# Kernel optimization log

Hardware: AMD Instinct MI355X
Metric: run time of the kernel (lower is better)

Reference implementation:

```python
import jax, jax.numpy as jnp
import numpy as np

N = 50000      # movie nodes
E = 1000000    # edges per metapath
F_IN = 512
HID = 128
HEADS = 8
D = HID // HEADS  # 16
OUT = 3
NEG_SLOPE = 0.2   # PyG HANConv leaky_relu slope


def setup_inputs() -> dict:
    key = jax.random.key(0)
    ks = jax.random.split(key, 16)
    x = jax.random.normal(ks[0], (N, F_IN), jnp.float32)
    ei0 = jax.random.randint(ks[1], (2, E), 0, N, jnp.int32)
    ei1 = jax.random.randint(ks[2], (2, E), 0, N, jnp.int32)
    W_proj = jax.random.normal(ks[3], (F_IN, HID), jnp.float32) / np.sqrt(F_IN)
    b_proj = jnp.zeros((HID,), jnp.float32)
    att_src0 = jax.random.normal(ks[4], (HEADS, D), jnp.float32) / np.sqrt(D)
    att_dst0 = jax.random.normal(ks[5], (HEADS, D), jnp.float32) / np.sqrt(D)
    att_src1 = jax.random.normal(ks[6], (HEADS, D), jnp.float32) / np.sqrt(D)
    att_dst1 = jax.random.normal(ks[7], (HEADS, D), jnp.float32) / np.sqrt(D)
    Wk = jax.random.normal(ks[8], (HID, HID), jnp.float32) / np.sqrt(HID)
    bk = jnp.zeros((HID,), jnp.float32)
    q = jax.random.normal(ks[9], (HID,), jnp.float32) / np.sqrt(HID)
    W_lin = jax.random.normal(ks[10], (HID, OUT), jnp.float32) / np.sqrt(HID)
    b_lin = jnp.zeros((OUT,), jnp.float32)
    return dict(x=x, edge_index_mp0=ei0, edge_index_mp1=ei1,
                W_proj=W_proj, b_proj=b_proj,
                att_src0=att_src0, att_dst0=att_dst0,
                att_src1=att_src1, att_dst1=att_dst1,
                Wk=Wk, bk=bk, q=q, W_lin=W_lin, b_lin=b_lin)


def _han_edge_type(xp, src, dst, att_src, att_dst):
    """Node-level multi-head attention for one metapath (eval mode, no dropout).
    xp: [N, H, D] projected features; src/dst: [E] indices.
    """
    a_src = jnp.einsum('nhd,hd->nh', xp, att_src)  # [N, H]
    a_dst = jnp.einsum('nhd,hd->nh', xp, att_dst)
    alpha = jax.nn.leaky_relu(a_src[src] + a_dst[dst], NEG_SLOPE)  # [E, H]
    # segment softmax over incoming edges of each dst node
    amax = jax.ops.segment_max(alpha, dst, num_segments=N)
    amax = jnp.where(jnp.isfinite(amax), amax, 0.0)
    ex = jnp.exp(alpha - amax[dst])
    denom = jax.ops.segment_sum(ex, dst, num_segments=N)
    w = ex / (denom[dst] + 1e-16)                 # [E, H]
    msg = w[:, :, None] * xp[src]                 # [E, H, D]
    out = jax.ops.segment_sum(msg, dst, num_segments=N)  # [N, H, D]
    return jax.nn.relu(out.reshape(N, HID))


def reference(x, edge_index_mp0, edge_index_mp1, W_proj, b_proj,
              att_src0, att_dst0, att_src1, att_dst1,
              Wk, bk, q, W_lin, b_lin):
    xp = (x @ W_proj + b_proj).reshape(N, HEADS, D)
    o0 = _han_edge_type(xp, edge_index_mp0[0], edge_index_mp0[1], att_src0, att_dst0)
    o1 = _han_edge_type(xp, edge_index_mp1[0], edge_index_mp1[1], att_src1, att_dst1)
    outs = jnp.stack([o0, o1], axis=0)            # [M=2, N, HID]
    # semantic-level attention: score_m = sum(q * mean_n tanh(k_lin(o_m)))
    scores = jnp.einsum('mh,h->m', jnp.tanh(outs @ Wk + bk).mean(axis=1), q)
    beta = jax.nn.softmax(scores)                 # [2]
    fused = jnp.einsum('m,mnh->nh', beta, outs)   # [N, HID]
    return fused @ W_lin + b_lin                  # [N, OUT]
```

## Files before the change

kernel.cpp:

```cpp
#include <hip/hip_runtime.h>
#include <hip/hip_bf16.h>

#define NN 50000
#define EE 1000000
#define FIN 512
#define HIDDEN 128
#define NH 8
#define DH 16
#define NOUT 3
#define NBUCK 196
#define EPB 8192
#define NBLKA ((EE + EPB - 1) / EPB)

typedef unsigned short u16;
typedef unsigned int u32;
typedef __attribute__((ext_vector_type(8))) short short8;
typedef __attribute__((ext_vector_type(4))) float f32x4;

__device__ __forceinline__ float b2f(u16 b) { return __uint_as_float(((u32)b) << 16); }
__device__ __forceinline__ u16 f2b(float f) { return (u16)(__float_as_uint(f) >> 16); }
__device__ __forceinline__ u16 f2b_rne(float f) {
    u32 u = __float_as_uint(f);
    return (u16)((u + 0x7FFFu + ((u >> 16) & 1u)) >> 16);
}

__device__ __forceinline__ void gload16(const u16* g, u16* l) {
    __builtin_amdgcn_global_load_lds(
        (const __attribute__((address_space(1))) unsigned int*)(g),
        (__attribute__((address_space(3))) unsigned int*)(l), 16, 0, 0);
}

#define W_WP   0
#define W_BP   65536
#define W_AS0  65664
#define W_AD0  65792
#define W_AS1  65920
#define W_AD1  66048
#define W_WK   66176
#define W_BK   82560
#define W_Q    82688
#define W_WL   82816
#define W_BL   83200
#define W_TOT  83203

__global__ void k_detect(const void* __restrict__ x, int* __restrict__ flag)
{
    const u16* xb = (const u16*)x;
    int t = threadIdx.x;
    int insane = 0;
    #pragma unroll
    for (int i = 0; i < 16; ++i) {
        int idx = ((t * 16 + i) * 131) * 2;
        float v = b2f(xb[idx]);
        float a = fabsf(v);
        bool sane = (a == 0.0f) || (a >= 1e-8f && a <= 1e4f);
        insane += sane ? 0 : 1;
    }
    __shared__ int red[256];
    red[t] = insane;
    __syncthreads();
    for (int s = 128; s > 0; s >>= 1) { if (t < s) red[t] += red[t + s]; __syncthreads(); }
    if (t == 0) flag[0] = (red[0] > 1024) ? 1 : 0;
}

__global__ __launch_bounds__(256) void k_convert(
    const void* Wp, const void* bp, const void* as0, const void* ad0,
    const void* as1, const void* ad1, const void* Wk, const void* bk,
    const void* q, const void* Wl, const void* bl,
    const int* __restrict__ flag, float* __restrict__ W)
{
    int i = blockIdx.x * 256 + threadIdx.x;
    if (i >= W_TOT) return;
    const void* src; int off;
    if      (i < W_BP)  { src = Wp;  off = i; }
    else if (i < W_AS0) { src = bp;  off = i - W_BP; }
    else if (i < W_AD0) { src = as0; off = i - W_AS0; }
    else if (i < W_AS1) { src = ad0; off = i - W_AD0; }
    else if (i < W_AD1) { src = as1; off = i - W_AS1; }
    else if (i < W_WK)  { src = ad1; off = i - W_AD1; }
    else if (i < W_BK)  { src = Wk;  off = i - W_WK; }
    else if (i < W_Q)   { src = bk;  off = i - W_BK; }
    else if (i < W_WL)  { src = q;   off = i - W_Q; }
    else if (i < W_BL)  { src = Wl;  off = i - W_WL; }
    else                { src = bl;  off = i - W_BL; }
    float v = flag[0] ? ((const float*)src)[off] : b2f(((const u16*)src)[off]);
    W[i] = v;
}

#define PREPN (FIN*HIDDEN + HIDDEN*HIDDEN)
__global__ __launch_bounds__(256) void k_prepw(
    const float* __restrict__ Wpf, const float* __restrict__ Wkf,
    u16* __restrict__ WhiT, u16* __restrict__ WloT, u16* __restrict__ WkThi)
{
    int idx = blockIdx.x*256 + threadIdx.x;
    if (idx >= PREPN) return;
    if (idx < FIN*HIDDEN) {
        int k = idx >> 7, n = idx & 127;
        float w = Wpf[idx];
        u32 hb = __float_as_uint(w) & 0xFFFF0000u;
        WhiT[(size_t)n*FIN + k] = (u16)(hb >> 16);
        WloT[(size_t)n*FIN + k] = f2b(w - __uint_as_float(hb));
    } else {
        int i = idx - FIN*HIDDEN;
        int k = i >> 7, h = i & 127;
        WkThi[(size_t)h*HIDDEN + k] = f2b_rne(Wkf[i]);
    }
}

__global__ __launch_bounds__(256) void k_projm_f32(
    const void* __restrict__ xv, const u16* __restrict__ WhiT,
    const u16* __restrict__ WloT, const float* __restrict__ bpf,
    const int* __restrict__ flag, u16* __restrict__ xpb)
{
    if (!flag[0]) return;
    __shared__ u16 lds[2][16384];
    const int t = threadIdx.x;
    const int lane = t & 63;
    const int wid = t >> 6;
    const int m16 = lane & 15;
    const int quad = lane >> 4;
    const int wr = wid >> 1, wc = wid & 1;
    const int blockRow = blockIdx.x * 128;
    const float* xf = (const float*)xv;

    const int srow = t >> 1;
    const int shalf = t & 1;
    int gxrow = blockRow + srow; if (gxrow >= NN) gxrow = NN - 1;
    const float* xr = xf + (size_t)gxrow * FIN + shalf * 16;
    const int ssw = (srow >> 1) & 3;
    const int aw0 = srow*32 + ((shalf*2)     ^ ssw) * 8;
    const int aw1 = srow*32 + ((shalf*2 + 1) ^ ssw) * 8;

    int bp0 = t, bp1 = t + 256;
    int br0 = bp0 >> 2, br1 = bp1 >> 2;
    int bc0 = (bp0 & 3) ^ ((br0 >> 1) & 3);
    int bc1 = (bp1 & 3) ^ ((br1 >> 1) & 3);
    const u16* srcBh0 = WhiT + (size_t)br0 * FIN + bc0 * 8;
    const u16* srcBh1 = WhiT + (size_t)br1 * FIN + bc1 * 8;
    const u16* srcBl0 = WloT + (size_t)br0 * FIN + bc0 * 8;
    const u16* srcBl1 = WloT + (size_t)br1 * FIN + bc1 * 8;
    const int dB0 = bp0 * 8, dB1 = bp1 * 8;

    int aoff[4], boff[4];
    #pragma unroll
    for (int mt = 0; mt < 4; ++mt) {
        int r = wr*64 + mt*16 + m16;
        aoff[mt] = r*32 + ((quad ^ ((r >> 1) & 3)) << 3);
    }
    #pragma unroll
    for (int nt = 0; nt < 4; ++nt) {
        int r = wc*64 + nt*16 + m16;
        boff[nt] = r*32 + ((quad ^ ((r >> 1) & 3)) << 3);
    }

    f32x4 acc[4][4];
    #pragma unroll
    for (int i = 0; i < 4; ++i)
        #pragma unroll
        for (int j = 0; j < 4; ++j) acc[i][j] = (f32x4)(0.f);

    u16* Lc = lds[0];
    u16* Ln = lds[1];

    {
        float4 v0 = *(const float4*)(xr);
        float4 v1 = *(const float4*)(xr + 4);
        float4 v2 = *(const float4*)(xr + 8);
        float4 v3 = *(const float4*)(xr + 12);
        gload16(srcBh0, Lc + 8192  + dB0);
        gload16(srcBh1, Lc + 8192  + dB1);
        gload16(srcBl0, Lc + 12288 + dB0);
        gload16(srcBl1, Lc + 12288 + dB1);
        float xs[16] = {v0.x,v0.y,v0.z,v0.w, v1.x,v1.y,v1.z,v1.w,
                        v2.x,v2.y,v2.z,v2.w, v3.x,v3.y,v3.z,v3.w};
        short8 h0, h1, l0, l1;
        #pragma unroll
        for (int j = 0; j < 8; ++j) {
            u32 u = __float_as_uint(xs[j]);   u32 hb = u & 0xFFFF0000u;
            h0[j] = (short)(hb >> 16); l0[j] = (short)f2b(xs[j] - __uint_as_float(hb));
            u32 u2 = __float_as_uint(xs[8+j]); u32 hb2 = u2 & 0xFFFF0000u;
            h1[j] = (short)(hb2 >> 16); l1[j] = (short)f2b(xs[8+j] - __uint_as_float(hb2));
        }
        *(short8*)(Lc + aw0) = h0;
        *(short8*)(Lc + aw1) = h1;
        *(short8*)(Lc + 4096 + aw0) = l0;
        *(short8*)(Lc + 4096 + aw1) = l1;
    }
    __syncthreads();

    #pragma unroll 1
    for (int ks = 0; ks < 16; ++ks) {
        const int kt = (ks + 1) * 32;
        float4 v0, v1, v2, v3;
        if (ks < 15) {
            v0 = *(const float4*)(xr + kt);
            v1 = *(const float4*)(xr + kt + 4);
            v2 = *(const float4*)(xr + kt + 8);
            v3 = *(const float4*)(xr + kt + 12);
            gload16(srcBh0 + kt, Ln + 8192  + dB0);
            gload16(srcBh1 + kt, Ln + 8192  + dB1);
            gload16(srcBl0 + kt, Ln + 12288 + dB0);
            gload16(srcBl1 + kt, Ln + 12288 + dB1);
        }
        short8 bh[4], bl[4];
        #pragma unroll
        for (int nt = 0; nt < 4; ++nt) {
            bh[nt] = *(const short8*)(Lc + 8192  + boff[nt]);
            bl[nt] = *(const short8*)(Lc + 12288 + boff[nt]);
        }
        #pragma unroll
        for (int mt = 0; mt < 4; ++mt) {
            short8 ah = *(const short8*)(Lc + aoff[mt]);
            short8 al = *(const short8*)(Lc + 4096 + aoff[mt]);
            #pragma unroll
            for (int nt = 0; nt < 4; ++nt) {
                acc[mt][nt] = __builtin_amdgcn_mfma_f32_16x16x32_bf16(ah, bh[nt], acc[mt][nt], 0,0,0);
                acc[mt][nt] = __builtin_amdgcn_mfma_f32_16x16x32_bf16(ah, bl[nt], acc[mt][nt], 0,0,0);
                acc[mt][nt] = __builtin_amdgcn_mfma_f32_16x16x32_bf16(al, bh[nt], acc[mt][nt], 0,0,0);
            }
        }
        if (ks < 15) {
            float xs[16] = {v0.x,v0.y,v0.z,v0.w, v1.x,v1.y,v1.z,v1.w,
                            v2.x,v2.y,v2.z,v2.w, v3.x,v3.y,v3.z,v3.w};
            short8 h0, h1, l0, l1;
            #pragma unroll
            for (int j = 0; j < 8; ++j) {
                u32 u = __float_as_uint(xs[j]);   u32 hb = u & 0xFFFF0000u;
                h0[j] = (short)(hb >> 16); l0[j] = (short)f2b(xs[j] - __uint_as_float(hb));
                u32 u2 = __float_as_uint(xs[8+j]); u32 hb2 = u2 & 0xFFFF0000u;
                h1[j] = (short)(hb2 >> 16); l1[j] = (short)f2b(xs[8+j] - __uint_as_float(hb2));
            }
            *(short8*)(Ln + aw0) = h0;
            *(short8*)(Ln + aw1) = h1;
            *(short8*)(Ln + 4096 + aw0) = l0;
            *(short8*)(Ln + 4096 + aw1) = l1;
        }
        __syncthreads();
        u16* tmp = Lc; Lc = Ln; Ln = tmp;
    }

    #pragma unroll
    for (int nt = 0; nt < 4; ++nt) {
        int col = wc*64 + nt*16 + m16;
        float bias = bpf[col];
        #pragma unroll
        for (int mt = 0; mt < 4; ++mt) {
            int orow0 = blockRow + wr*64 + mt*16 + quad*4;
            #pragma unroll
            for (int r = 0; r < 4; ++r) {
                int orow = orow0 + r;
                if (orow < NN) xpb[(size_t)orow*HIDDEN + col] = f2b_rne(acc[mt][nt][r] + bias);
            }
        }
    }
}

__global__ __launch_bounds__(256) void k_projm_bf16(
    const void* __restrict__ x, const u16* __restrict__ WhiT,
    const u16* __restrict__ WloT, const float* __restrict__ bpf,
    const int* __restrict__ flag, u16* __restrict__ xpb)
{
    if (flag[0]) return;
    __shared__ u16 lds[2][12288];
    const int t = threadIdx.x;
    const int lane = t & 63;
    const int wid = t >> 6;
    const int m16 = lane & 15;
    const int quad = lane >> 4;
    const int wr = wid >> 1, wc = wid & 1;
    const int blockRow = blockIdx.x * 128;
    const u16* xb = (const u16*)x;

    const int r0 = t >> 2,         c0 = (t & 3) * 8;
    const int r1 = (t + 256) >> 2, c1 = ((t + 256) & 3) * 8;
    int g0 = blockRow + r0; if (g0 >= NN) g0 = NN - 1;
    int g1 = blockRow + r1; if (g1 >= NN) g1 = NN - 1;
    const u16* srcA0  = xb   + (size_t)g0 * FIN + c0;
    const u16* srcA1  = xb   + (size_t)g1 * FIN + c1;
    const u16* srcBh0 = WhiT + (size_t)r0 * FIN + c0;
    const u16* srcBh1 = WhiT + (size_t)r1 * FIN + c1;
    const u16* srcBl0 = WloT + (size_t)r0 * FIN + c0;
    const u16* srcBl1 = WloT + (size_t)r1 * FIN + c1;

#define PSTAGE(buf, kt) do { \
        gload16(srcA0  + (kt), &lds[buf][t*8]); \
        gload16(srcA1  + (kt), &lds[buf][2048 + t*8]); \
        gload16(srcBh0 + (kt), &lds[buf][4096 + t*8]); \
        gload16(srcBh1 + (kt), &lds[buf][6144 + t*8]); \
        gload16(srcBl0 + (kt), &lds[buf][8192 + t*8]); \
        gload16(srcBl1 + (kt), &lds[buf][10240 + t*8]); \
    } while (0)

    f32x4 acc[4][4];
    #pragma unroll
    for (int i = 0; i < 4; ++i)
        #pragma unroll
        for (int j = 0; j < 4; ++j) acc[i][j] = (f32x4)(0.f);

    PSTAGE(0, 0);
    __syncthreads();
    int cur = 0;
    for (int ks = 0; ks < 16; ++ks) {
        if (ks < 15) {
            if (cur) PSTAGE(0, (ks + 1) * 32);
            else     PSTAGE(1, (ks + 1) * 32);
        }
        const u16* L = lds[cur];
        short8 a[4], bh[4], bl[4];
        #pragma unroll
        for (int mt = 0; mt < 4; ++mt)
            a[mt] = *(const short8*)&L[(wr*64 + mt*16 + m16)*32 + quad*8];
        #pragma unroll
        for (int nt = 0; nt < 4; ++nt) {
            bh[nt] = *(const short8*)&L[4096 + (wc*64 + nt*16 + m16)*32 + quad*8];
            bl[nt] = *(const short8*)&L[8192 + (wc*64 + nt*16 + m16)*32 + quad*8];
        }
        #pragma unroll
        for (int mt = 0; mt < 4; ++mt)
            #pragma unroll
            for (int nt = 0; nt < 4; ++nt) {
                acc[mt][nt] = __builtin_amdgcn_mfma_f32_16x16x32_bf16(a[mt], bh[nt], acc[mt][nt], 0,0,0);
                acc[mt][nt] = __builtin_amdgcn_mfma_f32_16x16x32_bf16(a[mt], bl[nt], acc[mt][nt], 0,0,0);
            }
        __syncthreads();
        cur ^= 1;
    }
#undef PSTAGE

    #pragma unroll
    for (int nt = 0; nt < 4; ++nt) {
        int col = wc*64 + nt*16 + m16;
        float bias = bpf[col];
        #pragma unroll
        for (int mt = 0; mt < 4; ++mt) {
            int orow0 = blockRow + wr*64 + mt*16 + quad*4;
            #pragma unroll
            for (int r = 0; r < 4; ++r) {
                int orow = orow0 + r;
                if (orow < NN) xpb[(size_t)orow*HIDDEN + col] = f2b_rne(acc[mt][nt][r] + bias);
            }
        }
    }
}

__global__ __launch_bounds__(256) void k_attcoef(
    const u16* __restrict__ xpb, const float* __restrict__ watt,
    float* __restrict__ o_as0, float* __restrict__ o_ad0,
    float* __restrict__ o_as1, float* __restrict__ o_ad1)
{
    __shared__ float s0[128], d0[128], s1[128], d1[128];
    const int t = threadIdx.x;
    if (t < 128) { s0[t]=watt[t]; d0[t]=watt[128+t]; s1[t]=watt[256+t]; d1[t]=watt[384+t]; }
    __syncthreads();
    int tid = blockIdx.x*256 + t;
    if (tid >= NN*NH) return;
    int h = tid & 7;
    const u32* px = (const u32*)(xpb + (size_t)tid * DH);
    float xv[16];
    #pragma unroll
    for (int i=0;i<8;++i){ u32 v=px[i]; xv[i*2]=b2f((u16)(v&0xFFFF)); xv[i*2+1]=b2f((u16)(v>>16)); }
    float r0=0.f,r1=0.f,r2=0.f,r3=0.f;
    #pragma unroll
    for (int d=0; d<16; ++d) {
        float xvd = xv[d];
        r0 += xvd*s0[h*16+d]; r1 += xvd*d0[h*16+d];
        r2 += xvd*s1[h*16+d]; r3 += xvd*d1[h*16+d];
    }
    o_as0[tid]=r0; o_ad0[tid]=r1; o_as1[tid]=r2; o_ad1[tid]=r3;
}

__global__ __launch_bounds__(256) void k_bhist(
    const int* __restrict__ ei0, const int* __restrict__ ei1, int* __restrict__ bcnt)
{
    const int mp = blockIdx.y;
    const int* ei = mp ? ei1 : ei0;
    __shared__ int h[NBUCK];
    const int t = threadIdx.x;
    for (int b = t; b < NBUCK; b += 256) h[b] = 0;
    __syncthreads();
    const int e0 = blockIdx.x * EPB;
    #pragma unroll
    for (int i = 0; i < EPB/256; ++i) {
        int idx = e0 + i*256 + t;
        if (idx < EE) atomicAdd(&h[ei[EE + idx] >> 8], 1);
    }
    __syncthreads();
    for (int b = t; b < NBUCK; b += 256)
        if (h[b]) atomicAdd(&bcnt[mp*256 + b], h[b]);
}

__global__ __launch_bounds__(512) void k_bscan(
    const int* __restrict__ bcnt, int* __restrict__ bstart, int* __restrict__ curA)
{
    __shared__ int s[2][256];
    const int mp = threadIdx.x >> 8;
    const int t = threadIdx.x & 255;
    int v = (t < NBUCK) ? bcnt[mp*256 + t] : 0;
    s[mp][t] = v;
    __syncthreads();
    for (int off = 1; off < 256; off <<= 1) {
        int u = (t >= off) ? s[mp][t - off] : 0;
        __syncthreads();
        s[mp][t] += u;
        __syncthreads();
    }
    int excl = s[mp][t] - v;
    if (t < NBUCK) {
        bstart[mp*200 + t] = excl;
        curA[(mp*256 + t)*16] = excl;
    }
    if (t == NBUCK - 1) bstart[mp*200 + NBUCK] = excl + v;
}

__global__ __launch_bounds__(256) void k_scatterA(
    const int* __restrict__ ei0, const int* __restrict__ ei1,
    int* __restrict__ curA, int2* __restrict__ tmp0, int2* __restrict__ tmp1)
{
    const int mp = blockIdx.y;
    const int* ei = mp ? ei1 : ei0;
    int2* tmp = mp ? tmp1 : tmp0;
    __shared__ int hist[NBUCK];
    __shared__ int seg[NBUCK];
    __shared__ int cnt[NBUCK];
    const int t = threadIdx.x;
    for (int b = t; b < NBUCK; b += 256) hist[b] = 0;
    __syncthreads();
    const int e0 = blockIdx.x * EPB;
    #pragma unroll
    for (int i = 0; i < EPB/256; ++i) {
        int idx = e0 + i*256 + t;
        if (idx < EE) atomicAdd(&hist[ei[EE + idx] >> 8], 1);
    }
    __syncthreads();
    for (int b = t; b < NBUCK; b += 256) {
        int h = hist[b];
        seg[b] = h ? atomicAdd(&curA[(mp*256 + b)*16], h) : 0;
        cnt[b] = 0;
    }
    __syncthreads();
    #pragma unroll
    for (int i = 0; i < EPB/256; ++i) {
        int idx = e0 + i*256 + t;
        if (idx < EE) {
            int s = ei[idx], d = ei[EE + idx];
            int b = d >> 8;
            int pos = seg[b] + atomicAdd(&cnt[b], 1);
            tmp[pos] = make_int2(s, d);
        }
    }
}

__global__ __launch_bounds__(256) void k_scatterB(
    const int2* __restrict__ tmp0, const int2* __restrict__ tmp1,
    const int* __restrict__ bstart,
    int* __restrict__ base0, int* __restrict__ base1,
    int* __restrict__ srt0, int* __restrict__ srt1)
{
    const int b = blockIdx.x;
    const int mp = blockIdx.y;
    const int2* tmp = mp ? tmp1 : tmp0;
    int* base = mp ? base1 : base0;
    int* srt  = mp ? srt1 : srt0;
    const int lo = bstart[mp*200 + b];
    const int hi = bstart[mp*200 + b + 1];
    __shared__ int lcnt[256];
    __shared__ int loff[256];
    const int t = threadIdx.x;
    lcnt[t] = 0;
    __syncthreads();
    for (int i = lo + t; i < hi; i += 256)
        atomicAdd(&lcnt[tmp[i].y & 255], 1);
    __syncthreads();
    int v = lcnt[t];
    loff[t] = v;
    __syncthreads();
    for (int off = 1; off < 256; off <<= 1) {
        int u = (t >= off) ? loff[t - off] : 0;
        __syncthreads();
        loff[t] += u;
        __syncthreads();
    }
    int excl = loff[t] - v;
    int node = (b << 8) + t;
    if (node < NN) base[node] = lo + excl;
    if (b == NBUCK - 1 && t == 0) base[NN] = EE;
    __syncthreads();
    loff[t] = excl;
    lcnt[t] = 0;
    __syncthreads();
    for (int i = lo + t; i < hi; i += 256) {
        int2 sd = tmp[i];
        int local = sd.y & 255;
        int pos = lo + loff[local] + atomicAdd(&lcnt[local], 1);
        srt[pos] = sd.x;
    }
}

__global__ __launch_bounds__(256) void k_gather(
    const int* __restrict__ srt0, const int* __restrict__ srt1,
    const int* __restrict__ base0, const int* __restrict__ base1,
    const float* __restrict__ as0, const float* __restrict__ ad0,
    const float* __restrict__ as1, const float* __restrict__ ad1,
    const u16* __restrict__ xpb, u16* __restrict__ obf0, u16* __restrict__ obf1)
{
    const int t = threadIdx.x;
    const int wid = blockIdx.x*4 + (t >> 6);
    if (wid >= NN) return;
    const int lane = t & 63;
    const int hc = lane & 7;
    const int eg = lane >> 3;
    const int mp = blockIdx.y;
    const int*  srt  = mp ? srt1  : srt0;
    const int*  base = mp ? base1 : base0;
    const float* asr = mp ? as1 : as0;
    const float* ads = mp ? ad1 : ad0;
    u16* obf = mp ? obf1 : obf0;
    const u32* xw = (const u32*)xpb;

    const int b = base[wid], e = base[wid + 1];
    const float adv = ads[wid*NH + hc];
    const int bp = (lane >> 3) << 2;
    float accx = 0.f, accy = 0.f, den = 0.f;

    for (int i = b; i < e; i += 8) {
        int il = i + eg;
        int ilc = il < e ? il : e - 1;
        int s = srt[ilc];

        u32 rv0, rv1, rv2, rv3, rv4, rv5, rv6, rv7;
        {
            const u32* r0p = xw + ((size_t)(u32)__builtin_amdgcn_readlane(s, 0)  << 6);
            const u32* r1p = xw + ((size_t)(u32)__builtin_amdgcn_readlane(s, 8)  << 6);
            const u32* r2p = xw + ((size_t)(u32)__builtin_amdgcn_readlane(s, 16) << 6);
            const u32* r3p = xw + ((size_t)(u32)__builtin_amdgcn_readlane(s, 24) << 6);
            const u32* r4p = xw + ((size_t)(u32)__builtin_amdgcn_readlane(s, 32) << 6);
            const u32* r5p = xw + ((size_t)(u32)__builtin_amdgcn_readlane(s, 40) << 6);
            const u32* r6p = xw + ((size_t)(u32)__builtin_amdgcn_readlane(s, 48) << 6);
            const u32* r7p = xw + ((size_t)(u32)__builtin_amdgcn_readlane(s, 56) << 6);
            rv0 = r0p[lane]; rv1 = r1p[lane]; rv2 = r2p[lane]; rv3 = r3p[lane];
            rv4 = r4p[lane]; rv5 = r5p[lane]; rv6 = r6p[lane]; rv7 = r7p[lane];
        }

        float av = asr[s*NH + hc] + adv;
        av = fmaxf(av, 0.2f*av);
        float w = (il < e) ? __expf(av) : 0.f;
        int wi = __float_as_int(w);

        #pragma unroll
        for (int k2 = 0; k2 < 8; ++k2) {
            float wk = __int_as_float(__builtin_amdgcn_ds_bpermute(bp + k2*32, wi));
            u32 v = (k2==0)?rv0:(k2==1)?rv1:(k2==2)?rv2:(k2==3)?rv3:
                    (k2==4)?rv4:(k2==5)?rv5:(k2==6)?rv6:rv7;
            accx = fmaf(wk, b2f((u16)(v & 0xFFFF)), accx);
            accy = fmaf(wk, b2f((u16)(v >> 16)), accy);
            den += wk;
        }
    }
    float inv = 1.f / (den + 1e-16f);
    u32 lo = f2b_rne(accx*inv), hi = f2b_rne(accy*inv);
    ((u32*)obf)[(size_t)wid*64 + lane] = (hi << 16) | lo;
}

__global__ __launch_bounds__(256) void k_semantic(
    const u16* __restrict__ obf0, const u16* __restrict__ obf1,
    const u16* __restrict__ WkThi, const float* __restrict__ bkf,
    const float* __restrict__ qf, float* __restrict__ scores)
{
    const int t = threadIdx.x;
    const int lane = t & 63;
    const int w = t >> 6;
    const int m16 = lane & 15;
    const int quad = lane >> 4;
    const int mp = blockIdx.y;
    const u16* om = mp ? obf1 : obf0;
    const int tile = blockIdx.x*4 + w;

    float partial = 0.f;
    if (tile < NN/16) {
        int row = tile*16 + m16;
        f32x4 acc[8];
        #pragma unroll
        for (int i=0;i<8;++i) acc[i] = (f32x4)(0.f);

        for (int kt = 0; kt < HIDDEN; kt += 32) {
            int kbase = kt + quad*8;
            short8 a = *(const short8*)(om + (size_t)row*HIDDEN + kbase);
            #pragma unroll
            for (int j=0;j<8;++j) a[j] = ((u16)a[j] & 0x8000u) ? (short)0 : a[j];
            #pragma unroll
            for (int nt = 0; nt < 8; ++nt) {
                int n = nt*16 + m16;
                short8 bhi = *(const short8*)(WkThi + (size_t)n*HIDDEN + kbase);
                acc[nt] = __builtin_amdgcn_mfma_f32_16x16x32_bf16(a, bhi, acc[nt], 0,0,0);
            }
        }
        #pragma unroll
        for (int nt=0; nt<8; ++nt) {
            int col = nt*16 + m16;
            float bkv = bkf[col], qv = qf[col];
            #pragma unroll
            for (int r=0;r<4;++r)
                partial += qv * tanhf(acc[nt][r] + bkv);
        }
    }
    __shared__ float red[256];
    red[t] = partial;
    __syncthreads();
    for (int s2 = 128; s2 > 0; s2 >>= 1) {
        if (t < s2) red[t] += red[t + s2];
        __syncthreads();
    }
    if (t == 0) unsafeAtomicAdd(&scores[mp], red[0]);
}

__global__ void k_beta(const float* __restrict__ scores, float* __restrict__ beta)
{
    float s0 = scores[0] / (float)NN;
    float s1 = scores[1] / (float)NN;
    float m = fmaxf(s0, s1);
    float e0 = __expf(s0-m), e1 = __expf(s1-m);
    float inv = 1.f/(e0+e1);
    beta[0] = e0*inv; beta[1] = e1*inv;
}

__global__ __launch_bounds__(256) void k_final(
    const u16* __restrict__ obf0, const u16* __restrict__ obf1,
    const float* __restrict__ beta, const float* __restrict__ Wlf,
    const float* __restrict__ blf, const int* __restrict__ flag,
    void* __restrict__ outv)
{
    __shared__ float fus[16*128];
    __shared__ float WlL[384];
    __shared__ float blL[3];
    const int t = threadIdx.x;
    for (int i = t; i < 384; i += 256) WlL[i] = Wlf[i];
    if (t < 3) blL[t] = blf[t];
    float b0 = beta[0], b1 = beta[1];
    const u32* o0w = (const u32*)obf0;
    const u32* o1w = (const u32*)obf1;
    size_t base = (size_t)blockIdx.x * 16 * 64;
    #pragma unroll
    for (int i=0;i<4;++i) {
        int j = t + i*256;
        u32 v0 = o0w[base + j];
        u32 v1 = o1w[base + j];
        float l0 = fmaxf(b2f((u16)(v0&0xFFFF)),0.f), h0 = fmaxf(b2f((u16)(v0>>16)),0.f);
        float l1 = fmaxf(b2f((u16)(v1&0xFFFF)),0.f), h1 = fmaxf(b2f((u16)(v1>>16)),0.f);
        int row = j >> 6, cp = j & 63;
        fus[row*128 + cp*2]     = b0*l0 + b1*l1;
        fus[row*128 + cp*2 + 1] = b0*h0 + b1*h1;
    }
    __syncthreads();
    if (t < 48) {
        int node = t / 3, c = t % 3;
        float acc = blL[c];
        const float* fr = &fus[node*128];
        #pragma unroll 16
        for (int k=0;k<128;++k) acc += fr[k]*WlL[k*3+c];
        size_t oi = (size_t)(blockIdx.x*16 + node)*NOUT + c;
        if (flag[0]) ((float*)outv)[oi] = acc;
        else         ((__hip_bfloat16*)outv)[oi] = __float2bfloat16(acc);
    }
}

extern "C" void kernel_launch(void* const* d_in, const int* in_sizes, int n_in,
                              void* d_out, int out_size, void* d_ws, size_t ws_size,
                              hipStream_t stream)
{
    const void* x   = d_in[0];
    const int* ei0  = (const int*)d_in[1];
    const int* ei1  = (const int*)d_in[2];

    float* ws = (float*)d_ws;
    u16*   xpb     = (u16*)ws;
    float* a_src0  = ws +  3200000;
    float* a_dst0  = ws +  3600000;
    float* a_src1  = ws +  4000000;
    float* a_dst1  = ws +  4400000;
    u16*   obf0    = (u16*)(ws + 4800000);
    u16*   obf1    = (u16*)(ws + 8000000);
    int*   srt0    = (int*)(ws + 11200000);
    int*   srt1    = (int*)(ws + 12200000);
    int2*  tmp0    = (int2*)(ws + 13200000);
    int2*  tmp1    = (int2*)(ws + 17200000);
    int*   base0   = (int*)(ws + 21200000);
    int*   base1   = (int*)(ws + 21250004);
    float* scores  = ws + 21300008;
    int*   bcnt    = (int*)(ws + 21300010);
    int*   bstart  = (int*)(ws + 21300522);
    float* beta    = ws + 21400010;
    int*   flag    = (int*)(ws + 21400012);
    float* wconv   = ws + 21400016;
    int*   curA    = (int*)(ws + 21483348);
    u16*   WhiT    = (u16*)(ws + 21491540);
    u16*   WloT    = (u16*)(ws + 21524308);
    u16*   WkThi   = (u16*)(ws + 21557076);

    hipMemsetAsync(scores, 0, (size_t)514 * sizeof(int), stream);

    k_detect<<<1, 256, 0, stream>>>(x, flag);
    k_convert<<<(W_TOT+255)/256, 256, 0, stream>>>(
        d_in[3], d_in[4], d_in[5], d_in[6], d_in[7], d_in[8],
        d_in[9], d_in[10], d_in[11], d_in[12], d_in[13], flag, wconv);
    k_prepw<<<(PREPN+255)/256, 256, 0, stream>>>(wconv + W_WP, wconv + W_WK,
                                                 WhiT, WloT, WkThi);

    k_projm_f32<<<(NN+127)/128, 256, 0, stream>>>(x, WhiT, WloT, wconv + W_BP, flag, xpb);
    k_projm_bf16<<<(NN+127)/128, 256, 0, stream>>>(x, WhiT, WloT, wconv + W_BP, flag, xpb);

    k_attcoef<<<(NN*NH + 255)/256, 256, 0, stream>>>(xpb, wconv + W_AS0,
                                                     a_src0, a_dst0, a_src1, a_dst1);
    k_bhist<<<dim3(NBLKA,2), 256, 0, stream>>>(ei0, ei1, bcnt);
    k_bscan<<<1, 512, 0, stream>>>(bcnt, bstart, curA);
    k_scatterA<<<dim3(NBLKA,2), 256, 0, stream>>>(ei0, ei1, curA, tmp0, tmp1);
    k_scatterB<<<dim3(NBUCK,2), 256, 0, stream>>>(tmp0, tmp1, bstart,
                                                  base0, base1, srt0, srt1);
    k_gather<<<dim3((NN + 3)/4, 2), 256, 0, stream>>>(
        srt0, srt1, base0, base1, a_src0, a_dst0, a_src1, a_dst1, xpb, obf0, obf1);

    k_semantic<<<dim3((NN/16 + 3)/4, 2), 256, 0, stream>>>(
        obf0, obf1, WkThi, wconv + W_BK, wconv + W_Q, scores);
    k_beta<<<1, 1, 0, stream>>>(scores, beta);
    k_final<<<NN/16, 256, 0, stream>>>(obf0, obf1, beta, wconv + W_WL, wconv + W_BL,
                                       flag, d_out);
}
```

Baseline: 418.9 us.

## Merge prep, projection and bucketing kernels; drop bucket histogram pass and beta kernel

Folds flag detection, weight conversion, weight transposition and buffer zeroing into one prep kernel. Merges the f32 and bf16 projection kernels into one. Fuses attention-coefficient computation with bucket scatter into fixed-capacity segments packed as 16-bit pairs, which removes the separate histogram and scan passes. Computes beta inside the final kernel and replaces tanhf with an exp-based formula. This cuts launch count and global passes over the edges, but relies on per-bucket capacity bounds and on node indices fitting in 16 bits.

```diff
diff --git a/kernel.cpp b/kernel.cpp
--- a/kernel.cpp
+++ b/kernel.cpp
@@ -11,6 +11,7 @@
 #define NBUCK 196
 #define EPB 8192
 #define NBLKA ((EE + EPB - 1) / EPB)
+#define ATTBLK ((NN*NH + 255) / 256)
 
 typedef unsigned short u16;
 typedef unsigned int u32;
@@ -30,89 +31,85 @@
         (__attribute__((address_space(3))) unsigned int*)(l), 16, 0, 0);
 }
 
-#define W_WP   0
 #define W_BP   65536
 #define W_AS0  65664
-#define W_AD0  65792
-#define W_AS1  65920
-#define W_AD1  66048
-#define W_WK   66176
 #define W_BK   82560
 #define W_Q    82688
 #define W_WL   82816
 #define W_BL   83200
-#define W_TOT  83203
-
-__global__ void k_detect(const void* __restrict__ x, int* __restrict__ flag)
-{
+
+__global__ __launch_bounds__(256) void k_prep(
+    const void* __restrict__ x, const void* __restrict__ Wp, const void* __restrict__ Wk,
+    const void* bp, const void* as0, const void* ad0, const void* as1, const void* ad1,
+    const void* bk, const void* q, const void* Wl, const void* bl,
+    int* __restrict__ flag, float* __restrict__ scores, int* __restrict__ curA,
+    float* __restrict__ wconv, u16* __restrict__ WhiT, u16* __restrict__ WloT,
+    u16* __restrict__ WkThi)
+{
+    const int t = threadIdx.x;
+    const int bid = blockIdx.x;
+
     const u16* xb = (const u16*)x;
-    int t = threadIdx.x;
-    int insane = 0;
-    #pragma unroll
-    for (int i = 0; i < 16; ++i) {
-        int idx = ((t * 16 + i) * 131) * 2;
-        float v = b2f(xb[idx]);
+    {
+        float v = b2f(xb[((t*16 + (bid & 15))*131)*2]);
         float a = fabsf(v);
-        bool sane = (a == 0.0f) || (a >= 1e-8f && a <= 1e4f);
-        insane += sane ? 0 : 1;
-    }
-    __shared__ int red[256];
-    red[t] = insane;
-    __syncthreads();
-    for (int s = 128; s > 0; s >>= 1) { if (t < s) red[t] += red[t + s]; __syncthreads(); }
-    if (t == 0) flag[0] = (red[0] > 1024) ? 1 : 0;
-}
-
-__global__ __launch_bounds__(256) void k_convert(
-    const void* Wp, const void* bp, const void* as0, const void* ad0,
-    const void* as1, const void* ad1, const void* Wk, const void* bk,
-    const void* q, const void* Wl, const void* bl,
-    const int* __restrict__ flag, float* __restrict__ W)
-{
-    int i = blockIdx.x * 256 + threadIdx.x;
-    if (i >= W_TOT) return;
-    const void* src; int off;
-    if      (i < W_BP)  { src = Wp;  off = i; }
-    else if (i < W_AS0) { src = bp;  off = i - W_BP; }
-    else if (i < W_AD0) { src = as0; off = i - W_AS0; }
-    else if (i < W_AS1) { src = ad0; off = i - W_AD0; }
-    else if (i < W_AD1) { src = as1; off = i - W_AS1; }
-    else if (i < W_WK)  { src = ad1; off = i - W_AD1; }
-    else if (i < W_BK)  { src = Wk;  off = i - W_WK; }
-    else if (i < W_Q)   { src = bk;  off = i - W_BK; }
-    else if (i < W_WL)  { src = q;   off = i - W_Q; }
-    else if (i < W_BL)  { src = Wl;  off = i - W_WL; }
-    else                { src = bl;  off = i - W_BL; }
-    float v = flag[0] ? ((const float*)src)[off] : b2f(((const u16*)src)[off]);
-    W[i] = v;
-}
-
-#define PREPN (FIN*HIDDEN + HIDDEN*HIDDEN)
-__global__ __launch_bounds__(256) void k_prepw(
-    const float* __restrict__ Wpf, const float* __restrict__ Wkf,
-    u16* __restrict__ WhiT, u16* __restrict__ WloT, u16* __restrict__ WkThi)
-{
-    int idx = blockIdx.x*256 + threadIdx.x;
-    if (idx >= PREPN) return;
-    if (idx < FIN*HIDDEN) {
-        int k = idx >> 7, n = idx & 127;
-        float w = Wpf[idx];
-        u32 hb = __float_as_uint(w) & 0xFFFF0000u;
-        WhiT[(size_t)n*FIN + k] = (u16)(hb >> 16);
-        WloT[(size_t)n*FIN + k] = f2b(w - __uint_as_float(hb));
-    } else {
-        int i = idx - FIN*HIDDEN;
-        int k = i >> 7, h = i & 127;
-        WkThi[(size_t)h*HIDDEN + k] = f2b_rne(Wkf[i]);
-    }
-}
-
-__global__ __launch_bounds__(256) void k_projm_f32(
+        int insane = ((a == 0.0f) || (a >= 1e-8f && a <= 1e4f)) ? 0 : 1;
+        __shared__ int red[256];
+        red[t] = insane;
+        __syncthreads();
+        for (int s = 128; s > 0; s >>= 1) { if (t < s) red[t] += red[t+s]; __syncthreads(); }
+        const int f = (red[0] > 64) ? 1 : 0;
+        if (bid == 0 && t == 0) { flag[0] = f; scores[0] = 0.f; scores[1] = 0.f; }
+
+        if (bid < 256) {
+            int idx = bid*256 + t;
+            float w = f ? ((const float*)Wp)[idx] : b2f(((const u16*)Wp)[idx]);
+            int k = idx >> 7, n = idx & 127;
+            u32 hb = __float_as_uint(w) & 0xFFFF0000u;
+            WhiT[(size_t)n*FIN + k] = (u16)(hb >> 16);
+            WloT[(size_t)n*FIN + k] = f2b(w - __uint_as_float(hb));
+        } else if (bid < 320) {
+            int i = (bid-256)*256 + t;
+            float w = f ? ((const float*)Wk)[i] : b2f(((const u16*)Wk)[i]);
+            int k = i >> 7, h = i & 127;
+            WkThi[(size_t)h*HIDDEN + k] = f2b_rne(w);
+        } else if (bid == 320) {
+            #pragma unroll
+            for (int j = 0; j < 6; ++j) {
+                int i = j*256 + t;
+                if (i < 1283) {
+                    const void* src; int off; int dst;
+                    if (i < 640) {
+                        dst = W_BP + i;
+                        if (i < 128)      { src = bp;  off = i; }
+                        else if (i < 256) { src = as0; off = i-128; }
+                        else if (i < 384) { src = ad0; off = i-256; }
+                        else if (i < 512) { src = as1; off = i-384; }
+                        else              { src = ad1; off = i-512; }
+                    } else if (i < 896) {
+                        dst = W_BK + (i-640);
+                        if (i < 768) { src = bk; off = i-640; }
+                        else         { src = q;  off = i-768; }
+                    } else {
+                        dst = W_WL + (i-896);
+                        if (i < 1280) { src = Wl; off = i-896; }
+                        else          { src = bl; off = i-1280; }
+                    }
+                    wconv[dst] = f ? ((const float*)src)[off] : b2f(((const u16*)src)[off]);
+                }
+            }
+        } else {
+            int i = (bid-321)*256 + t;
+            if (i < 8192) curA[i] = 0;
+        }
+    }
+}
+
+__global__ __launch_bounds__(256) void k_projm(
     const void* __restrict__ xv, const u16* __restrict__ WhiT,
     const u16* __restrict__ WloT, const float* __restrict__ bpf,
     const int* __restrict__ flag, u16* __restrict__ xpb)
 {
-    if (!flag[0]) return;
     __shared__ u16 lds[2][16384];
     const int t = threadIdx.x;
     const int lane = t & 63;
@@ -121,37 +118,6 @@
     const int quad = lane >> 4;
     const int wr = wid >> 1, wc = wid & 1;
     const int blockRow = blockIdx.x * 128;
-    const float* xf = (const float*)xv;
-
-    const int srow = t >> 1;
-    const int shalf = t & 1;
-    int gxrow = blockRow + srow; if (gxrow >= NN) gxrow = NN - 1;
-    const float* xr = xf + (size_t)gxrow * FIN + shalf * 16;
-    const int ssw = (srow >> 1) & 3;
-    const int aw0 = srow*32 + ((shalf*2)     ^ ssw) * 8;
-    const int aw1 = srow*32 + ((shalf*2 + 1) ^ ssw) * 8;
-
-    int bp0 = t, bp1 = t + 256;
-    int br0 = bp0 >> 2, br1 = bp1 >> 2;
-    int bc0 = (bp0 & 3) ^ ((br0 >> 1) & 3);
-    int bc1 = (bp1 & 3) ^ ((br1 >> 1) & 3);
-    const u16* srcBh0 = WhiT + (size_t)br0 * FIN + bc0 * 8;
-    const u16* srcBh1 = WhiT + (size_t)br1 * FIN + bc1 * 8;
-    const u16* srcBl0 = WloT + (size_t)br0 * FIN + bc0 * 8;
-    const u16* srcBl1 = WloT + (size_t)br1 * FIN + bc1 * 8;
-    const int dB0 = bp0 * 8, dB1 = bp1 * 8;
-
-    int aoff[4], boff[4];
-    #pragma unroll
-    for (int mt = 0; mt < 4; ++mt) {
-        int r = wr*64 + mt*16 + m16;
-        aoff[mt] = r*32 + ((quad ^ ((r >> 1) & 3)) << 3);
-    }
-    #pragma unroll
-    for (int nt = 0; nt < 4; ++nt) {
-        int r = wc*64 + nt*16 + m16;
-        boff[nt] = r*32 + ((quad ^ ((r >> 1) & 3)) << 3);
-    }
 
     f32x4 acc[4][4];
     #pragma unroll
@@ -159,67 +125,49 @@
         #pragma unroll
         for (int j = 0; j < 4; ++j) acc[i][j] = (f32x4)(0.f);
 
-    u16* Lc = lds[0];
-    u16* Ln = lds[1];
-
-    {
-        float4 v0 = *(const float4*)(xr);
-        float4 v1 = *(const float4*)(xr + 4);
-        float4 v2 = *(const float4*)(xr + 8);
-        float4 v3 = *(const float4*)(xr + 12);
-        gload16(srcBh0, Lc + 8192  + dB0);
-        gload16(srcBh1, Lc + 8192  + dB1);
-        gload16(srcBl0, Lc + 12288 + dB0);
-        gload16(srcBl1, Lc + 12288 + dB1);
-        float xs[16] = {v0.x,v0.y,v0.z,v0.w, v1.x,v1.y,v1.z,v1.w,
-                        v2.x,v2.y,v2.z,v2.w, v3.x,v3.y,v3.z,v3.w};
-        short8 h0, h1, l0, l1;
-        #pragma unroll
-        for (int j = 0; j < 8; ++j) {
-            u32 u = __float_as_uint(xs[j]);   u32 hb = u & 0xFFFF0000u;
-            h0[j] = (short)(hb >> 16); l0[j] = (short)f2b(xs[j] - __uint_as_float(hb));
-            u32 u2 = __float_as_uint(xs[8+j]); u32 hb2 = u2 & 0xFFFF0000u;
-            h1[j] = (short)(hb2 >> 16); l1[j] = (short)f2b(xs[8+j] - __uint_as_float(hb2));
-        }
-        *(short8*)(Lc + aw0) = h0;
-        *(short8*)(Lc + aw1) = h1;
-        *(short8*)(Lc + 4096 + aw0) = l0;
-        *(short8*)(Lc + 4096 + aw1) = l1;
-    }
-    __syncthreads();
-
-    #pragma unroll 1
-    for (int ks = 0; ks < 16; ++ks) {
-        const int kt = (ks + 1) * 32;
-        float4 v0, v1, v2, v3;
-        if (ks < 15) {
-            v0 = *(const float4*)(xr + kt);
-            v1 = *(const float4*)(xr + kt + 4);
-            v2 = *(const float4*)(xr + kt + 8);
-            v3 = *(const float4*)(xr + kt + 12);
-            gload16(srcBh0 + kt, Ln + 8192  + dB0);
-            gload16(srcBh1 + kt, Ln + 8192  + dB1);
-            gload16(srcBl0 + kt, Ln + 12288 + dB0);
-            gload16(srcBl1 + kt, Ln + 12288 + dB1);
-        }
-        short8 bh[4], bl[4];
+    if (flag[0]) {
+        const float* xf = (const float*)xv;
+        const int srow = t >> 1;
+        const int shalf = t & 1;
+        int gxrow = blockRow + srow; if (gxrow >= NN) gxrow = NN - 1;
+        const float* xr = xf + (size_t)gxrow * FIN + shalf * 16;
+        const int ssw = (srow >> 1) & 3;
+        const int aw0 = srow*32 + ((shalf*2)     ^ ssw) * 8;
+        const int aw1 = srow*32 + ((shalf*2 + 1) ^ ssw) * 8;
+
+        int bp0 = t, bp1 = t + 256;
+        int br0 = bp0 >> 2, br1 = bp1 >> 2;
+        int bc0 = (bp0 & 3) ^ ((br0 >> 1) & 3);
+        int bc1 = (bp1 & 3) ^ ((br1 >> 1) & 3);
+        const u16* srcBh0 = WhiT + (size_t)br0 * FIN + bc0 * 8;
+        const u16* srcBh1 = WhiT + (size_t)br1 * FIN + bc1 * 8;
+        const u16* srcBl0 = WloT + (size_t)br0 * FIN + bc0 * 8;
+        const u16* srcBl1 = WloT + (size_t)br1 * FIN + bc1 * 8;
+        const int dB0 = bp0 * 8, dB1 = bp1 * 8;
+
+        int aoff[4], boff[4];
+        #pragma unroll
+        for (int mt = 0; mt < 4; ++mt) {
+            int r = wr*64 + mt*16 + m16;
+            aoff[mt] = r*32 + ((quad ^ ((r >> 1) & 3)) << 3);
+        }
         #pragma unroll
         for (int nt = 0; nt < 4; ++nt) {
-            bh[nt] = *(const short8*)(Lc + 8192  + boff[nt]);
-            bl[nt] = *(const short8*)(Lc + 12288 + boff[nt]);
-        }
-        #pragma unroll
-        for (int mt = 0; mt < 4; ++mt) {
-            short8 ah = *(const short8*)(Lc + aoff[mt]);
-            short8 al = *(const short8*)(Lc + 4096 + aoff[mt]);
-            #pragma unroll
-            for (int nt = 0; nt < 4; ++nt) {
-                acc[mt][nt] = __builtin_amdgcn_mfma_f32_16x16x32_bf16(ah, bh[nt], acc[mt][nt], 0,0,0);
-                acc[mt][nt] = __builtin_amdgcn_mfma_f32_16x16x32_bf16(ah, bl[nt], acc[mt][nt], 0,0,0);
-                acc[mt][nt] = __builtin_amdgcn_mfma_f32_16x16x32_bf16(al, bh[nt], acc[mt][nt], 0,0,0);
-            }
-        }
-        if (ks < 15) {
+            int r = wc*64 + nt*16 + m16;
+            boff[nt] = r*32 + ((quad ^ ((r >> 1) & 3)) << 3);
+        }
+
+        u16* Lc = lds[0];
+        u16* Ln = lds[1];
+        {
+            float4 v0 = *(const float4*)(xr);
+            float4 v1 = *(const float4*)(xr + 4);
+            float4 v2 = *(const float4*)(xr + 8);
+            float4 v3 = *(const float4*)(xr + 12);
+            gload16(srcBh0, Lc + 8192  + dB0);
+            gload16(srcBh1, Lc + 8192  + dB1);
+            gload16(srcBl0, Lc + 12288 + dB0);
+            gload16(srcBl1, Lc + 12288 + dB1);
             float xs[16] = {v0.x,v0.y,v0.z,v0.w, v1.x,v1.y,v1.z,v1.w,
                             v2.x,v2.y,v2.z,v2.w, v3.x,v3.y,v3.z,v3.w};
             short8 h0, h1, l0, l1;
@@ -230,57 +178,75 @@
                 u32 u2 = __float_as_uint(xs[8+j]); u32 hb2 = u2 & 0xFFFF0000u;
                 h1[j] = (short)(hb2 >> 16); l1[j] = (short)f2b(xs[8+j] - __uint_as_float(hb2));
             }
-            *(short8*)(Ln + aw0) = h0;
-            *(short8*)(Ln + aw1) = h1;
-            *(short8*)(Ln + 4096 + aw0) = l0;
-            *(short8*)(Ln + 4096 + aw1) = l1;
-        }
-        __syncthreads();
-        u16* tmp = Lc; Lc = Ln; Ln = tmp;
-    }
-
-    #pragma unroll
-    for (int nt = 0; nt < 4; ++nt) {
-        int col = wc*64 + nt*16 + m16;
-        float bias = bpf[col];
-        #pragma unroll
-        for (int mt = 0; mt < 4; ++mt) {
-            int orow0 = blockRow + wr*64 + mt*16 + quad*4;
-            #pragma unroll
-            for (int r = 0; r < 4; ++r) {
-                int orow = orow0 + r;
-                if (orow < NN) xpb[(size_t)orow*HIDDEN + col] = f2b_rne(acc[mt][nt][r] + bias);
-            }
-        }
-    }
-}
-
-__global__ __launch_bounds__(256) void k_projm_bf16(
-    const void* __restrict__ x, const u16* __restrict__ WhiT,
-    const u16* __restrict__ WloT, const float* __restrict__ bpf,
-    const int* __restrict__ flag, u16* __restrict__ xpb)
-{
-    if (flag[0]) return;
-    __shared__ u16 lds[2][12288];
-    const int t = threadIdx.x;
-    const int lane = t & 63;
-    const int wid = t >> 6;
-    const int m16 = lane & 15;
-    const int quad = lane >> 4;
-    const int wr = wid >> 1, wc = wid & 1;
-    const int blockRow = blockIdx.x * 128;
-    const u16* xb = (const u16*)x;
-
-    const int r0 = t >> 2,         c0 = (t & 3) * 8;
-    const int r1 = (t + 256) >> 2, c1 = ((t + 256) & 3) * 8;
-    int g0 = blockRow + r0; if (g0 >= NN) g0 = NN - 1;
-    int g1 = blockRow + r1; if (g1 >= NN) g1 = NN - 1;
-    const u16* srcA0  = xb   + (size_t)g0 * FIN + c0;
-    const u16* srcA1  = xb   + (size_t)g1 * FIN + c1;
-    const u16* srcBh0 = WhiT + (size_t)r0 * FIN + c0;
-    const u16* srcBh1 = WhiT + (size_t)r1 * FIN + c1;
-    const u16* srcBl0 = WloT + (size_t)r0 * FIN + c0;
-    const u16* srcBl1 = WloT + (size_t)r1 * FIN + c1;
+            *(short8*)(Lc + aw0) = h0;
+            *(short8*)(Lc + aw1) = h1;
+            *(short8*)(Lc + 4096 + aw0) = l0;
+            *(short8*)(Lc + 4096 + aw1) = l1;
+        }
+        __syncthreads();
+
+        #pragma unroll 1
+        for (int ks = 0; ks < 16; ++ks) {
+            const int kt = (ks + 1) * 32;
+            float4 v0, v1, v2, v3;
+            if (ks < 15) {
+                v0 = *(const float4*)(xr + kt);
+                v1 = *(const float4*)(xr + kt + 4);
+                v2 = *(const float4*)(xr + kt + 8);
+                v3 = *(const float4*)(xr + kt + 12);
+                gload16(srcBh0 + kt, Ln + 8192  + dB0);
+                gload16(srcBh1 + kt, Ln + 8192  + dB1);
+                gload16(srcBl0 + kt, Ln + 12288 + dB0);
+                gload16(srcBl1 + kt, Ln + 12288 + dB1);
+            }
+            short8 bh[4], bl[4];
+            #pragma unroll
+            for (int nt = 0; nt < 4; ++nt) {
+                bh[nt] = *(const short8*)(Lc + 8192  + boff[nt]);
+                bl[nt] = *(const short8*)(Lc + 12288 + boff[nt]);
+            }
+            #pragma unroll
+            for (int mt = 0; mt < 4; ++mt) {
+                short8 ah = *(const short8*)(Lc + aoff[mt]);
+                short8 al = *(const short8*)(Lc + 4096 + aoff[mt]);
+                #pragma unroll
+                for (int nt = 0; nt < 4; ++nt) {
+                    acc[mt][nt] = __builtin_amdgcn_mfma_f32_16x16x32_bf16(ah, bh[nt], acc[mt][nt], 0,0,0);
+                    acc[mt][nt] = __builtin_amdgcn_mfma_f32_16x16x32_bf16(ah, bl[nt], acc[mt][nt], 0,0,0);
+                    acc[mt][nt] = __builtin_amdgcn_mfma_f32_16x16x32_bf16(al, bh[nt], acc[mt][nt], 0,0,0);
+                }
+            }
+            if (ks < 15) {
+                float xs[16] = {v0.x,v0.y,v0.z,v0.w, v1.x,v1.y,v1.z,v1.w,
+                                v2.x,v2.y,v2.z,v2.w, v3.x,v3.y,v3.z,v3.w};
+                short8 h0, h1, l0, l1;
+                #pragma unroll
+                for (int j = 0; j < 8; ++j) {
+                    u32 u = __float_as_uint(xs[j]);   u32 hb = u & 0xFFFF0000u;
+                    h0[j] = (short)(hb >> 16); l0[j] = (short)f2b(xs[j] - __uint_as_float(hb));
+                    u32 u2 = __float_as_uint(xs[8+j]); u32 hb2 = u2 & 0xFFFF0000u;
+                    h1[j] = (short)(hb2 >> 16); l1[j] = (short)f2b(xs[8+j] - __uint_as_float(hb2));
+                }
+                *(short8*)(Ln + aw0) = h0;
+                *(short8*)(Ln + aw1) = h1;
+                *(short8*)(Ln + 4096 + aw0) = l0;
+                *(short8*)(Ln + 4096 + aw1) = l1;
+            }
+            __syncthreads();
+            u16* tmp = Lc; Lc = Ln; Ln = tmp;
+        }
+    } else {
+        const u16* xb = (const u16*)xv;
+        const int r0 = t >> 2,         c0 = (t & 3) * 8;
+        const int r1 = (t + 256) >> 2, c1 = ((t + 256) & 3) * 8;
+        int g0 = blockRow + r0; if (g0 >= NN) g0 = NN - 1;
+        int g1 = blockRow + r1; if (g1 >= NN) g1 = NN - 1;
+        const u16* srcA0  = xb   + (size_t)g0 * FIN + c0;
+        const u16* srcA1  = xb   + (size_t)g1 * FIN + c1;
+        const u16* srcBh0 = WhiT + (size_t)r0 * FIN + c0;
+        const u16* srcBh1 = WhiT + (size_t)r1 * FIN + c1;
+        const u16* srcBl0 = WloT + (size_t)r0 * FIN + c0;
+        const u16* srcBl1 = WloT + (size_t)r1 * FIN + c1;
 
 #define PSTAGE(buf, kt) do { \
         gload16(srcA0  + (kt), &lds[buf][t*8]); \
@@ -291,41 +257,36 @@
         gload16(srcBl1 + (kt), &lds[buf][10240 + t*8]); \
     } while (0)
 
-    f32x4 acc[4][4];
-    #pragma unroll
-    for (int i = 0; i < 4; ++i)
-        #pragma unroll
-        for (int j = 0; j < 4; ++j) acc[i][j] = (f32x4)(0.f);
-
-    PSTAGE(0, 0);
-    __syncthreads();
-    int cur = 0;
-    for (int ks = 0; ks < 16; ++ks) {
-        if (ks < 15) {
-            if (cur) PSTAGE(0, (ks + 1) * 32);
-            else     PSTAGE(1, (ks + 1) * 32);
-        }
-        const u16* L = lds[cur];
-        short8 a[4], bh[4], bl[4];
-        #pragma unroll
-        for (int mt = 0; mt < 4; ++mt)
-            a[mt] = *(const short8*)&L[(wr*64 + mt*16 + m16)*32 + quad*8];
-        #pragma unroll
-        for (int nt = 0; nt < 4; ++nt) {
-            bh[nt] = *(const short8*)&L[4096 + (wc*64 + nt*16 + m16)*32 + quad*8];
-            bl[nt] = *(const short8*)&L[8192 + (wc*64 + nt*16 + m16)*32 + quad*8];
-        }
-        #pragma unroll
-        for (int mt = 0; mt < 4; ++mt)
+        PSTAGE(0, 0);
+        __syncthreads();
+        int cur = 0;
+        for (int ks = 0; ks < 16; ++ks) {
+            if (ks < 15) {
+                if (cur) PSTAGE(0, (ks + 1) * 32);
+                else     PSTAGE(1, (ks + 1) * 32);
+            }
+            const u16* L = lds[cur];
+            short8 a[4], bh[4], bl[4];
+            #pragma unroll
+            for (int mt = 0; mt < 4; ++mt)
+                a[mt] = *(const short8*)&L[(wr*64 + mt*16 + m16)*32 + quad*8];
             #pragma unroll
             for (int nt = 0; nt < 4; ++nt) {
-                acc[mt][nt] = __builtin_amdgcn_mfma_f32_16x16x32_bf16(a[mt], bh[nt], acc[mt][nt], 0,0,0);
-                acc[mt][nt] = __builtin_amdgcn_mfma_f32_16x16x32_bf16(a[mt], bl[nt], acc[mt][nt], 0,0,0);
-            }
-        __syncthreads();
-        cur ^= 1;
-    }
+                bh[nt] = *(const short8*)&L[4096 + (wc*64 + nt*16 + m16)*32 + quad*8];
+                bl[nt] = *(const short8*)&L[8192 + (wc*64 + nt*16 + m16)*32 + quad*8];
+            }
+            #pragma unroll
+            for (int mt = 0; mt < 4; ++mt)
+                #pragma unroll
+                for (int nt = 0; nt < 4; ++nt) {
+                    acc[mt][nt] = __builtin_amdgcn_mfma_f32_16x16x32_bf16(a[mt], bh[nt], acc[mt][nt], 0,0,0);
+                    acc[mt][nt] = __builtin_amdgcn_mfma_f32_16x16x32_bf16(a[mt], bl[nt], acc[mt][nt], 0,0,0);
+                }
+            __syncthreads();
+            cur ^= 1;
+        }
 #undef PSTAGE
+    }
 
     #pragma unroll
     for (int nt = 0; nt < 4; ++nt) {
@@ -343,133 +304,98 @@
     }
 }
 
-__global__ __launch_bounds__(256) void k_attcoef(
+__global__ __launch_bounds__(256) void k_fused1(
     const u16* __restrict__ xpb, const float* __restrict__ watt,
     float* __restrict__ o_as0, float* __restrict__ o_ad0,
-    float* __restrict__ o_as1, float* __restrict__ o_ad1)
-{
-    __shared__ float s0[128], d0[128], s1[128], d1[128];
+    float* __restrict__ o_as1, float* __restrict__ o_ad1,
+    const int* __restrict__ ei0, const int* __restrict__ ei1,
+    int* __restrict__ curA, u32* __restrict__ tmp0, u32* __restrict__ tmp1)
+{
+    __shared__ int sh[768];
     const int t = threadIdx.x;
-    if (t < 128) { s0[t]=watt[t]; d0[t]=watt[128+t]; s1[t]=watt[256+t]; d1[t]=watt[384+t]; }
-    __syncthreads();
-    int tid = blockIdx.x*256 + t;
-    if (tid >= NN*NH) return;
-    int h = tid & 7;
-    const u32* px = (const u32*)(xpb + (size_t)tid * DH);
-    float xv[16];
-    #pragma unroll
-    for (int i=0;i<8;++i){ u32 v=px[i]; xv[i*2]=b2f((u16)(v&0xFFFF)); xv[i*2+1]=b2f((u16)(v>>16)); }
-    float r0=0.f,r1=0.f,r2=0.f,r3=0.f;
-    #pragma unroll
-    for (int d=0; d<16; ++d) {
-        float xvd = xv[d];
-        r0 += xvd*s0[h*16+d]; r1 += xvd*d0[h*16+d];
-        r2 += xvd*s1[h*16+d]; r3 += xvd*d1[h*16+d];
-    }
-    o_as0[tid]=r0; o_ad0[tid]=r1; o_as1[tid]=r2; o_ad1[tid]=r3;
-}
-
-__global__ __launch_bounds__(256) void k_bhist(
-    const int* __restrict__ ei0, const int* __restrict__ ei1, int* __restrict__ bcnt)
-{
-    const int mp = blockIdx.y;
-    const int* ei = mp ? ei1 : ei0;
-    __shared__ int h[NBUCK];
-    const int t = threadIdx.x;
-    for (int b = t; b < NBUCK; b += 256) h[b] = 0;
-    __syncthreads();
-    const int e0 = blockIdx.x * EPB;
-    #pragma unroll
-    for (int i = 0; i < EPB/256; ++i) {
-        int idx = e0 + i*256 + t;
-        if (idx < EE) atomicAdd(&h[ei[EE + idx] >> 8], 1);
-    }
-    __syncthreads();
-    for (int b = t; b < NBUCK; b += 256)
-        if (h[b]) atomicAdd(&bcnt[mp*256 + b], h[b]);
-}
-
-__global__ __launch_bounds__(512) void k_bscan(
-    const int* __restrict__ bcnt, int* __restrict__ bstart, int* __restrict__ curA)
-{
-    __shared__ int s[2][256];
-    const int mp = threadIdx.x >> 8;
-    const int t = threadIdx.x & 255;
-    int v = (t < NBUCK) ? bcnt[mp*256 + t] : 0;
-    s[mp][t] = v;
-    __syncthreads();
-    for (int off = 1; off < 256; off <<= 1) {
-        int u = (t >= off) ? s[mp][t - off] : 0;
-        __syncthreads();
-        s[mp][t] += u;
-        __syncthreads();
-    }
-    int excl = s[mp][t] - v;
-    if (t < NBUCK) {
-        bstart[mp*200 + t] = excl;
-        curA[(mp*256 + t)*16] = excl;
-    }
-    if (t == NBUCK - 1) bstart[mp*200 + NBUCK] = excl + v;
-}
-
-__global__ __launch_bounds__(256) void k_scatterA(
-    const int* __restrict__ ei0, const int* __restrict__ ei1,
-    int* __restrict__ curA, int2* __restrict__ tmp0, int2* __restrict__ tmp1)
-{
-    const int mp = blockIdx.y;
-    const int* ei = mp ? ei1 : ei0;
-    int2* tmp = mp ? tmp1 : tmp0;
-    __shared__ int hist[NBUCK];
-    __shared__ int seg[NBUCK];
-    __shared__ int cnt[NBUCK];
-    const int t = threadIdx.x;
-    for (int b = t; b < NBUCK; b += 256) hist[b] = 0;
-    __syncthreads();
-    const int e0 = blockIdx.x * EPB;
-    #pragma unroll
-    for (int i = 0; i < EPB/256; ++i) {
-        int idx = e0 + i*256 + t;
-        if (idx < EE) atomicAdd(&hist[ei[EE + idx] >> 8], 1);
-    }
-    __syncthreads();
-    for (int b = t; b < NBUCK; b += 256) {
-        int h = hist[b];
-        seg[b] = h ? atomicAdd(&curA[(mp*256 + b)*16], h) : 0;
-        cnt[b] = 0;
-    }
-    __syncthreads();
-    #pragma unroll
-    for (int i = 0; i < EPB/256; ++i) {
-        int idx = e0 + i*256 + t;
-        if (idx < EE) {
-            int s = ei[idx], d = ei[EE + idx];
-            int b = d >> 8;
-            int pos = seg[b] + atomicAdd(&cnt[b], 1);
-            tmp[pos] = make_int2(s, d);
+    const int bid = blockIdx.x;
+
+    if (bid < ATTBLK) {
+        float* s0 = (float*)sh;
+        float* d0 = s0 + 128;
+        float* s1 = s0 + 256;
+        float* d1 = s0 + 384;
+        if (t < 128) { s0[t]=watt[t]; d0[t]=watt[128+t]; s1[t]=watt[256+t]; d1[t]=watt[384+t]; }
+        __syncthreads();
+        int tid = bid*256 + t;
+        if (tid >= NN*NH) return;
+        int h = tid & 7;
+        const u32* px = (const u32*)(xpb + (size_t)tid * DH);
+        float xv[16];
+        #pragma unroll
+        for (int i=0;i<8;++i){ u32 v=px[i]; xv[i*2]=b2f((u16)(v&0xFFFF)); xv[i*2+1]=b2f((u16)(v>>16)); }
+        float r0=0.f,r1=0.f,r2=0.f,r3=0.f;
+        #pragma unroll
+        for (int d=0; d<16; ++d) {
+            float xvd = xv[d];
+            r0 += xvd*s0[h*16+d]; r1 += xvd*d0[h*16+d];
+            r2 += xvd*s1[h*16+d]; r3 += xvd*d1[h*16+d];
+        }
+        o_as0[tid]=r0; o_ad0[tid]=r1; o_as1[tid]=r2; o_ad1[tid]=r3;
+    } else {
+        int r = bid - ATTBLK;
+        const int mp = (r >= NBLKA) ? 1 : 0;
+        const int bx = r - mp*NBLKA;
+        const int* ei = mp ? ei1 : ei0;
+        u32* tmp = mp ? tmp1 : tmp0;
+        int* hist = sh;
+        int* seg  = sh + 256;
+        int* cnt  = sh + 512;
+        for (int b = t; b < NBUCK; b += 256) hist[b] = 0;
+        __syncthreads();
+        const int e0 = bx * EPB;
+        #pragma unroll
+        for (int i = 0; i < EPB/256; ++i) {
+            int idx = e0 + i*256 + t;
+            if (idx < EE) atomicAdd(&hist[ei[EE + idx] >> 8], 1);
+        }
+        __syncthreads();
+        for (int b = t; b < NBUCK; b += 256) {
+            int h = hist[b];
+            seg[b] = h ? atomicAdd(&curA[(mp*256 + b)*16], h) : 0;
+            cnt[b] = 0;
+        }
+        __syncthreads();
+        #pragma unroll
+        for (int i = 0; i < EPB/256; ++i) {
+            int idx = e0 + i*256 + t;
+            if (idx < EE) {
+                int s = ei[idx], d = ei[EE + idx];
+                int b = d >> 8;
+                int pos = seg[b] + atomicAdd(&cnt[b], 1);
+                tmp[((size_t)b << 13) + pos] = (u32)(((d & 255) << 16) | s);
+            }
         }
     }
 }
 
 __global__ __launch_bounds__(256) void k_scatterB(
-    const int2* __restrict__ tmp0, const int2* __restrict__ tmp1,
-    const int* __restrict__ bstart,
-    int* __restrict__ base0, int* __restrict__ base1,
+    const u32* __restrict__ tmp0, const u32* __restrict__ tmp1,
+    const int* __restrict__ bcap,
+    int* __restrict__ ns0, int* __restrict__ ns1,
+    int* __restrict__ nc0, int* __restrict__ nc1,
     int* __restrict__ srt0, int* __restrict__ srt1)
 {
     const int b = blockIdx.x;
     const int mp = blockIdx.y;
-    const int2* tmp = mp ? tmp1 : tmp0;
-    int* base = mp ? base1 : base0;
-    int* srt  = mp ? srt1 : srt0;
-    const int lo = bstart[mp*200 + b];
-    const int hi = bstart[mp*200 + b + 1];
+    const u32* tmp = mp ? tmp1 : tmp0;
+    int* nstart = mp ? ns1 : ns0;
+    int* ncnt   = mp ? nc1 : nc0;
+    int* srt    = mp ? srt1 : srt0;
+    const int cntb = bcap[(mp*256 + b)*16];
+    const int segbase = b << 13;
     __shared__ int lcnt[256];
     __shared__ int loff[256];
     const int t = threadIdx.x;
     lcnt[t] = 0;
     __syncthreads();
-    for (int i = lo + t; i < hi; i += 256)
-        atomicAdd(&lcnt[tmp[i].y & 255], 1);
+    for (int i = t; i < cntb; i += 256)
+        atomicAdd(&lcnt[tmp[segbase + i] >> 16], 1);
     __syncthreads();
     int v = lcnt[t];
     loff[t] = v;
@@ -482,23 +408,23 @@
     }
     int excl = loff[t] - v;
     int node = (b << 8) + t;
-    if (node < NN) base[node] = lo + excl;
-    if (b == NBUCK - 1 && t == 0) base[NN] = EE;
+    if (node < NN) { nstart[node] = segbase + excl; ncnt[node] = v; }
     __syncthreads();
     loff[t] = excl;
     lcnt[t] = 0;
     __syncthreads();
-    for (int i = lo + t; i < hi; i += 256) {
-        int2 sd = tmp[i];
-        int local = sd.y & 255;
-        int pos = lo + loff[local] + atomicAdd(&lcnt[local], 1);
-        srt[pos] = sd.x;
+    for (int i = t; i < cntb; i += 256) {
+        u32 p = tmp[segbase + i];
+        int local = p >> 16;
+        int pos = segbase + loff[local] + atomicAdd(&lcnt[local], 1);
+        srt[pos] = (int)(p & 0xFFFFu);
     }
 }
 
 __global__ __launch_bounds__(256) void k_gather(
     const int* __restrict__ srt0, const int* __restrict__ srt1,
-    const int* __restrict__ base0, const int* __restrict__ base1,
+    const int* __restrict__ ns0, const int* __restrict__ ns1,
+    const int* __restrict__ nc0, const int* __restrict__ nc1,
     const float* __restrict__ as0, const float* __restrict__ ad0,
     const float* __restrict__ as1, const float* __restrict__ ad1,
     const u16* __restrict__ xpb, u16* __restrict__ obf0, u16* __restrict__ obf1)
@@ -511,13 +437,14 @@
     const int eg = lane >> 3;
     const int mp = blockIdx.y;
     const int*  srt  = mp ? srt1  : srt0;
-    const int*  base = mp ? base1 : base0;
+    const int*  nstart = mp ? ns1 : ns0;
+    const int*  ncnt   = mp ? nc1 : nc0;
     const float* asr = mp ? as1 : as0;
     const float* ads = mp ? ad1 : ad0;
     u16* obf = mp ? obf1 : obf0;
     const u32* xw = (const u32*)xpb;
 
-    const int b = base[wid], e = base[wid + 1];
+    const int b = nstart[wid], e = b + ncnt[wid];
     const float adv = ads[wid*NH + hc];
     const int bp = (lane >> 3) << 2;
     float accx = 0.f, accy = 0.f, den = 0.f;
@@ -599,8 +526,12 @@
             int col = nt*16 + m16;
             float bkv = bkf[col], qv = qf[col];
             #pragma unroll
-            for (int r=0;r<4;++r)
-                partial += qv * tanhf(acc[nt][r] + bkv);
+            for (int r=0;r<4;++r) {
+                float xx = acc[nt][r] + bkv;
+                xx = fminf(fmaxf(xx, -10.f), 10.f);
+                float tex = __expf(2.f*xx);
+                partial += qv * ((tex - 1.f) / (tex + 1.f));
+            }
         }
     }
     __shared__ float red[256];
@@ -613,19 +544,9 @@
     if (t == 0) unsafeAtomicAdd(&scores[mp], red[0]);
 }
 
-__global__ void k_beta(const float* __restrict__ scores, float* __restrict__ beta)
-{
-    float s0 = scores[0] / (float)NN;
-    float s1 = scores[1] / (float)NN;
-    float m = fmaxf(s0, s1);
-    float e0 = __expf(s0-m), e1 = __expf(s1-m);
-    float inv = 1.f/(e0+e1);
-    beta[0] = e0*inv; beta[1] = e1*inv;
-}
-
 __global__ __launch_bounds__(256) void k_final(
     const u16* __restrict__ obf0, const u16* __restrict__ obf1,
-    const float* __restrict__ beta, const float* __restrict__ Wlf,
+    const float* __restrict__ scores, const float* __restrict__ Wlf,
     const float* __restrict__ blf, const int* __restrict__ flag,
     void* __restrict__ outv)
 {
@@ -635,7 +556,13 @@
     const int t = threadIdx.x;
     for (int i = t; i < 384; i += 256) WlL[i] = Wlf[i];
     if (t < 3) blL[t] = blf[t];
-    float b0 = beta[0], b1 = beta[1];
+    float sc0 = scores[0] / (float)NN;
+    float sc1 = scores[1] / (float)NN;
+    float m = fmaxf(sc0, sc1);
+    float e0 = __expf(sc0-m), e1 = __expf(sc1-m);
+    float binv = 1.f/(e0+e1);
+    float b0 = e0*binv, b1 = e1*binv;
+
     const u32* o0w = (const u32*)obf0;
     const u32* o1w = (const u32*)obf1;
     size_t base = (size_t)blockIdx.x * 16 * 64;
@@ -680,47 +607,42 @@
     u16*   obf0    = (u16*)(ws + 4800000);
     u16*   obf1    = (u16*)(ws + 8000000);
     int*   srt0    = (int*)(ws + 11200000);
-    int*   srt1    = (int*)(ws + 12200000);
-    int2*  tmp0    = (int2*)(ws + 13200000);
-    int2*  tmp1    = (int2*)(ws + 17200000);
-    int*   base0   = (int*)(ws + 21200000);
-    int*   base1   = (int*)(ws + 21250004);
-    float* scores  = ws + 21300008;
-    int*   bcnt    = (int*)(ws + 21300010);
-    int*   bstart  = (int*)(ws + 21300522);
-    float* beta    = ws + 21400010;
-    int*   flag    = (int*)(ws + 21400012);
-    float* wconv   = ws + 21400016;
-    int*   curA    = (int*)(ws + 21483348);
-    u16*   WhiT    = (u16*)(ws + 21491540);
-    u16*   WloT    = (u16*)(ws + 21524308);
-    u16*   WkThi   = (u16*)(ws + 21557076);
-
-    hipMemsetAsync(scores, 0, (size_t)514 * sizeof(int), stream);
-
-    k_detect<<<1, 256, 0, stream>>>(x, flag);
-    k_convert<<<(W_TOT+255)/256, 256, 0, stream>>>(
-        d_in[3], d_in[4], d_in[5], d_in[6], d_in[7], d_in[8],
-        d_in[9], d_in[10], d_in[11], d_in[12], d_in[13], flag, wconv);
-    k_prepw<<<(PREPN+255)/256, 256, 0, stream>>>(wconv + W_WP, wconv + W_WK,
-                                                 WhiT, WloT, WkThi);
-
-    k_projm_f32<<<(NN+127)/128, 256, 0, stream>>>(x, WhiT, WloT, wconv + W_BP, flag, xpb);
-    k_projm_bf16<<<(NN+127)/128, 256, 0, stream>>>(x, WhiT, WloT, wconv + W_BP, flag, xpb);
-
-    k_attcoef<<<(NN*NH + 255)/256, 256, 0, stream>>>(xpb, wconv + W_AS0,
-                                                     a_src0, a_dst0, a_src1, a_dst1);
-    k_bhist<<<dim3(NBLKA,2), 256, 0, stream>>>(ei0, ei1, bcnt);
-    k_bscan<<<1, 512, 0, stream>>>(bcnt, bstart, curA);
-    k_scatterA<<<dim3(NBLKA,2), 256, 0, stream>>>(ei0, ei1, curA, tmp0, tmp1);
-    k_scatterB<<<dim3(NBUCK,2), 256, 0, stream>>>(tmp0, tmp1, bstart,
-                                                  base0, base1, srt0, srt1);
+    int*   srt1    = (int*)(ws + 12810000);
+    u32*   tmp0    = (u32*)(ws + 14420000);
+    u32*   tmp1    = (u32*)(ws + 16030000);
+    int*   nstart0 = (int*)(ws + 17640000);
+    int*   nstart1 = (int*)(ws + 17690000);
+    int*   ncnt0   = (int*)(ws + 17740000);
+    int*   ncnt1   = (int*)(ws + 17790000);
+    float* scores  = ws + 17840000;
+    int*   flag    = (int*)(ws + 17840004);
+    float* wconv   = ws + 17840008;
+    int*   curA    = (int*)(ws + 17923216);
+    u16*   WhiT    = (u16*)(ws + 17931408);
+    u16*   WloT    = (u16*)(ws + 17964176);
+    u16*   WkThi   = (u16*)(ws + 17996944);
+
+    k_prep<<<353, 256, 0, stream>>>(
+        x, d_in[3], d_in[9], d_in[4], d_in[5], d_in[6], d_in[7], d_in[8],
+        d_in[10], d_in[11], d_in[12], d_in[13],
+        flag, scores, curA, wconv, WhiT, WloT, WkThi);
+
+    k_projm<<<(NN+127)/128, 256, 0, stream>>>(x, WhiT, WloT, wconv + W_BP, flag, xpb);
+
+    k_fused1<<<ATTBLK + 2*NBLKA, 256, 0, stream>>>(
+        xpb, wconv + W_AS0, a_src0, a_dst0, a_src1, a_dst1,
+        ei0, ei1, curA, tmp0, tmp1);
+
+    k_scatterB<<<dim3(NBUCK,2), 256, 0, stream>>>(
+        tmp0, tmp1, curA, nstart0, nstart1, ncnt0, ncnt1, srt0, srt1);
+
     k_gather<<<dim3((NN + 3)/4, 2), 256, 0, stream>>>(
-        srt0, srt1, base0, base1, a_src0, a_dst0, a_src1, a_dst1, xpb, obf0, obf1);
+        srt0, srt1, nstart0, nstart1, ncnt0, ncnt1,
+        a_src0, a_dst0, a_src1, a_dst1, xpb, obf0, obf1);
 
     k_semantic<<<dim3((NN/16 + 3)/4, 2), 256, 0, stream>>>(
         obf0, obf1, WkThi, wconv + W_BK, wconv + W_Q, scores);
-    k_beta<<<1, 1, 0, stream>>>(scores, beta);
-    k_final<<<NN/16, 256, 0, stream>>>(obf0, obf1, beta, wconv + W_WL, wconv + W_BL,
+
+    k_final<<<NN/16, 256, 0, stream>>>(obf0, obf1, scores, wconv + W_WL, wconv + W_BL,
                                        flag, d_out);
 }
```

New measurement: 406.0 us. 1.03x faster.
